# Kernel optimization log

Measured on AMD Instinct MI355X. Metric: run time of the kernel, lower is better.

Reference implementation:

```python
import jax, jax.numpy as jnp
import numpy as np

A, B, K, P, STRIDE, ITERS = 32, 32, 3, 4, 2, 3
PSIZE = P * P
EPS = 1e-8


def add_patches(x):
    # x: (b, h, w, A*PSIZE) -> (b*oh*ow, K*K*A, PSIZE)
    b, h, w, c = x.shape
    oh = (h - K) // STRIDE + 1
    ow = (w - K) // STRIDE + 1
    idx = jnp.arange(oh) * STRIDE  # same for w since h == w here
    idx = idx[:, None] + jnp.arange(K)[None, :]          # (oh, K)
    p = x[:, idx]                                        # (b, oh, K, w, c)
    p = p[:, :, :, idx]                                  # (b, oh, K, ow, K, c)
    p = jnp.transpose(p, (0, 1, 3, 2, 4, 5))             # (b, oh, ow, K, K, c)
    p = p.reshape(b * oh * ow, K * K * A, PSIZE)
    return p, oh, ow


def transform_view(p_in, weights):
    # p_in: (N, K*K*A, PSIZE); weights: (K*K*A, B, P, P)
    N = p_in.shape[0]
    x = p_in.reshape(N, K * K * A, P, P)
    # pose matmul per (input capsule i, output type j): x[n,i] @ w[i,j]
    v = jnp.einsum('nipr,ijrq->nijpq', x, weights)       # (N, KKA, B, P, P)
    return v.reshape(N, K * K * A, B, PSIZE)


def squash(p):
    n2 = jnp.sum(p * p, axis=-1, keepdims=True)
    return p * n2 / (1.0 + n2) / jnp.sqrt(n2 + EPS)


def dynamic_routing(v, iters):
    # v: (N, KKA, B, PSIZE); inverted dynamic routing: softmax over input capsules
    N, KKA, Bt, _ = v.shape
    logits = jnp.zeros((N, KKA, Bt, 1), dtype=v.dtype)
    p = None
    for i in range(iters):
        r = jax.nn.softmax(logits, axis=1)               # route over input capsules
        p = squash(jnp.sum(r * v, axis=1, keepdims=True))  # (N,1,B,PSIZE)
        if i < iters - 1:
            logits = logits + jnp.sum(v * p, axis=-1, keepdims=True)
    return p[:, 0]                                       # (N, B, PSIZE)


def setup_inputs() -> dict:
    key = jax.random.key(0)
    k1, k2 = jax.random.split(key)
    x = jax.random.normal(k1, (2, 32, 32, A * PSIZE), dtype=jnp.float32)
    weights = jax.random.normal(k2, (K * K * A, B, P, P), dtype=jnp.float32)
    return {"x": x, "weights": weights}


def reference(x, weights):
    b = x.shape[0]
    p_in, oh, ow = add_patches(x)
    v = transform_view(p_in, weights)                    # (b*oh*ow, KKA, B, PSIZE)
    p_out = dynamic_routing(v, ITERS)                    # (b*oh*ow, B, PSIZE)
    return p_out.reshape(b, oh, ow, B * PSIZE)
```

## Files before the change

### kernel.cpp

```cpp
#include <hip/hip_runtime.h>


#define OH 15
#define OW 15
#define NITERS 3
#define EPS_ 1e-8f

#define XT_ELEMS (2 * 32 * 32 * 512)
#define WT_ELEMS (32 * 5 * 64 * 16)

typedef float v2f __attribute__((ext_vector_type(2)));

__device__ __forceinline__ v2f pfma(float a, v2f b, v2f c) {
    return __builtin_elementwise_fma((v2f){a, a}, b, c);
}
__device__ __forceinline__ float b_lo(unsigned int u) {
    union { unsigned int i; float f; } c; c.i = u << 16; return c.f;
}
__device__ __forceinline__ float b_hi(unsigned int u) {
    union { unsigned int i; float f; } c; c.i = u & 0xFFFF0000u; return c.f;
}
__device__ __forceinline__ unsigned short f2bf(float f) {
    union { float f; unsigned int i; } c; c.f = f;
    return (unsigned short)((c.i + 0x7FFFu + ((c.i >> 16) & 1u)) >> 16);
}

__global__ __launch_bounds__(256) void cast_x_kernel(
    const float* __restrict__ x, unsigned short* __restrict__ xt)
{
    const int tid = blockIdx.x * 256 + threadIdx.x;
    xt[tid] = f2bf(x[tid]);
}

__global__ __launch_bounds__(256) void permute_w_kernel(
    const float* __restrict__ w, unsigned short* __restrict__ wt)
{
    const int tid = blockIdx.x * 256 + threadIdx.x;
    const int j  = tid / 5120;
    const int r  = tid - j * 5120;
    const int k  = r >> 10;
    const int L  = (r >> 4) & 63;
    const int e  = r & 15;
    const int i  = L + 64 * k;
    wt[tid] = (i < 288) ? f2bf(w[(size_t)i * 512 + j * 16 + e]) : (unsigned short)0;
}

template <bool PERM>
__global__ __launch_bounds__(64, 3) void convcaps_kernel(
    const void* __restrict__ xp,
    const void* __restrict__ wp_,
    float* __restrict__ out)
{
    const int blk  = blockIdx.x;
    const int n    = blk >> 5;
    const int j    = blk & 31;
    const int lane = threadIdx.x;

    const int batch = n / (OH * OW);
    const int rem   = n - batch * OH * OW;
    const int oy    = rem / OW;
    const int ox    = rem - oy * OW;

    const bool has5 = (lane < 32);

    v2f v[5][8];
    float logit[5] = {0.f, 0.f, 0.f, 0.f, 0.f};

#pragma unroll
    for (int k = 0; k < 5; ++k) {
        if (k == 4 && !has5) {
#pragma unroll
            for (int m = 0; m < 8; ++m) v[4][m] = (v2f){0.f, 0.f};
        } else {
            const int i  = lane + 64 * k;
            const int a  = i & 31;
            const int kw = (i >> 5) % 3;
            const int kh = i / 96;
            const int h  = oy * 2 + kh;
            const int wc = ox * 2 + kw;
            const int pixel = (batch * 32 + h) * 32 + wc;

            float xr[16];
            v2f wr2[4][2];
            if (PERM) {
                const uint4* xb = reinterpret_cast<const uint4*>(
                    (const unsigned short*)xp + ((size_t)pixel * 512 + a * 16));
                uint4 u0 = xb[0], u1 = xb[1];
                xr[0]=b_lo(u0.x); xr[1]=b_hi(u0.x); xr[2]=b_lo(u0.y); xr[3]=b_hi(u0.y);
                xr[4]=b_lo(u0.z); xr[5]=b_hi(u0.z); xr[6]=b_lo(u0.w); xr[7]=b_hi(u0.w);
                xr[8]=b_lo(u1.x); xr[9]=b_hi(u1.x); xr[10]=b_lo(u1.y); xr[11]=b_hi(u1.y);
                xr[12]=b_lo(u1.z); xr[13]=b_hi(u1.z); xr[14]=b_lo(u1.w); xr[15]=b_hi(u1.w);
                const uint4* wb = reinterpret_cast<const uint4*>(
                    (const unsigned short*)wp_ + (((size_t)j * 5 + k) * 64 + lane) * 16);
                uint4 q0 = wb[0], q1 = wb[1];
                wr2[0][0] = (v2f){b_lo(q0.x), b_hi(q0.x)};
                wr2[0][1] = (v2f){b_lo(q0.y), b_hi(q0.y)};
                wr2[1][0] = (v2f){b_lo(q0.z), b_hi(q0.z)};
                wr2[1][1] = (v2f){b_lo(q0.w), b_hi(q0.w)};
                wr2[2][0] = (v2f){b_lo(q1.x), b_hi(q1.x)};
                wr2[2][1] = (v2f){b_lo(q1.y), b_hi(q1.y)};
                wr2[3][0] = (v2f){b_lo(q1.z), b_hi(q1.z)};
                wr2[3][1] = (v2f){b_lo(q1.w), b_hi(q1.w)};
            } else {
                const float4* xv = reinterpret_cast<const float4*>(
                    (const float*)xp + ((size_t)pixel * 512 + a * 16));
                float4 x0 = xv[0], x1 = xv[1], x2 = xv[2], x3 = xv[3];
                float t_[16] = { x0.x,x0.y,x0.z,x0.w, x1.x,x1.y,x1.z,x1.w,
                                 x2.x,x2.y,x2.z,x2.w, x3.x,x3.y,x3.z,x3.w };
#pragma unroll
                for (int e = 0; e < 16; ++e) xr[e] = t_[e];
                const float4* wq = reinterpret_cast<const float4*>(
                    (const float*)wp_ + ((size_t)i * 32 + j) * 16);
                float4 w0 = wq[0], w1 = wq[1], w2 = wq[2], w3 = wq[3];
                wr2[0][0]=(v2f){w0.x,w0.y}; wr2[0][1]=(v2f){w0.z,w0.w};
                wr2[1][0]=(v2f){w1.x,w1.y}; wr2[1][1]=(v2f){w1.z,w1.w};
                wr2[2][0]=(v2f){w2.x,w2.y}; wr2[2][1]=(v2f){w2.z,w2.w};
                wr2[3][0]=(v2f){w3.x,w3.y}; wr2[3][1]=(v2f){w3.z,w3.w};
            }

#pragma unroll
            for (int p = 0; p < 4; ++p) {
#pragma unroll
                for (int qq = 0; qq < 2; ++qq) {
                    v2f acc = (v2f){0.f, 0.f};
                    acc = pfma(xr[p*4+0], wr2[0][qq], acc);
                    acc = pfma(xr[p*4+1], wr2[1][qq], acc);
                    acc = pfma(xr[p*4+2], wr2[2][qq], acc);
                    acc = pfma(xr[p*4+3], wr2[3][qq], acc);
                    v[k][p*2+qq] = acc;
                }
            }
        }
    }

#pragma unroll
    for (int it = 0; it < NITERS; ++it) {
        v2f c2[8];
        float se_loc;
        if (it == 0) {
#pragma unroll
            for (int m = 0; m < 8; ++m)
                c2[m] = v[0][m] + v[1][m] + v[2][m] + v[3][m] + v[4][m];
            se_loc = 0.f;
        } else {
            const float e0 = __expf(logit[0]), e1 = __expf(logit[1]);
            const float e2 = __expf(logit[2]), e3 = __expf(logit[3]);
            const float e4 = __expf(logit[4]);
#pragma unroll
            for (int m = 0; m < 8; ++m)
                c2[m] = pfma(e0, v[0][m],
                        pfma(e1, v[1][m],
                        pfma(e2, v[2][m],
                        pfma(e3, v[3][m],
                        pfma(e4, v[4][m], (v2f){0.f, 0.f})))));
            se_loc = e0 + e1 + e2 + e3 + (has5 ? e4 : 0.f);
        }

        float c[16];
#pragma unroll
        for (int m = 0; m < 8; ++m) { c[2*m] = c2[m].x; c[2*m+1] = c2[m].y; }

        float seR = se_loc;
        float s8[8];
        {
            const bool b = lane & 1;
#pragma unroll
            for (int m = 0; m < 8; ++m) {
                float send = b ? c[2*m]   : c[2*m+1];
                float keep = b ? c[2*m+1] : c[2*m];
                s8[m] = keep + __shfl_xor(send, 1);
            }
            seR += __shfl_xor(seR, 1);
        }
        float s4[4];
        {
            const bool b = (lane >> 1) & 1;
#pragma unroll
            for (int m = 0; m < 4; ++m) {
                float send = b ? s8[2*m]   : s8[2*m+1];
                float keep = b ? s8[2*m+1] : s8[2*m];
                s4[m] = keep + __shfl_xor(send, 2);
            }
            seR += __shfl_xor(seR, 2);
        }
        float s2v[2];
        {
            const bool b = (lane >> 2) & 1;
#pragma unroll
            for (int m = 0; m < 2; ++m) {
                float send = b ? s4[2*m]   : s4[2*m+1];
                float keep = b ? s4[2*m+1] : s4[2*m];
                s2v[m] = keep + __shfl_xor(send, 4);
            }
            seR += __shfl_xor(seR, 4);
        }
        float s1;
        {
            const bool b = (lane >> 3) & 1;
            float send = b ? s2v[0] : s2v[1];
            float keep = b ? s2v[1] : s2v[0];
            s1 = keep + __shfl_xor(send, 8);
            seR += __shfl_xor(seR, 8);
        }
        s1 += __shfl_xor(s1, 16);  seR += __shfl_xor(seR, 16);
        s1 += __shfl_xor(s1, 32);  seR += __shfl_xor(seR, 32);

        const float s = (it == 0) ? s1 * (1.0f / 288.0f) : s1 / seR;

        float t2 = s * s;
        t2 += __shfl_xor(t2, 1);
        t2 += __shfl_xor(t2, 2);
        t2 += __shfl_xor(t2, 4);
        t2 += __shfl_xor(t2, 8);
        const float n2 = t2;
        const float scale = n2 / ((1.0f + n2) * sqrtf(n2 + EPS_));
        const float pval = s * scale;

        if (it < NITERS - 1) {
            float p[16];
#pragma unroll
            for (int q = 0; q < 16; ++q) p[q] = __shfl(pval, q);
            v2f p2[8];
#pragma unroll
            for (int m = 0; m < 8; ++m) p2[m] = (v2f){p[2*m], p[2*m+1]};
#pragma unroll
            for (int k = 0; k < 5; ++k) {
                v2f acc = (v2f){0.f, 0.f};
#pragma unroll
                for (int m = 0; m < 8; ++m)
                    acc = __builtin_elementwise_fma(v[k][m], p2[m], acc);
                logit[k] += acc.x + acc.y;
            }
        } else {
            if (lane < 16)
                out[(size_t)n * 512 + j * 16 + lane] = pval;
        }
    }
}

extern "C" void kernel_launch(void* const* d_in, const int* in_sizes, int n_in,
                              void* d_out, int out_size, void* d_ws, size_t ws_size,
                              hipStream_t stream) {
    const float* x = (const float*)d_in[0];
    const float* w = (const float*)d_in[1];
    float* out = (float*)d_out;
    const int nblocks = 450 * 32;

    const size_t need = (size_t)(XT_ELEMS + WT_ELEMS) * sizeof(unsigned short);
    if (d_ws != nullptr && ws_size >= need) {
        unsigned short* xt = (unsigned short*)d_ws;
        unsigned short* wt = xt + XT_ELEMS;
        cast_x_kernel<<<XT_ELEMS / 256, 256, 0, stream>>>(x, xt);
        permute_w_kernel<<<WT_ELEMS / 256, 256, 0, stream>>>(w, wt);
        convcaps_kernel<true><<<nblocks, 64, 0, stream>>>(xt, wt, out);
    } else {
        convcaps_kernel<false><<<nblocks, 64, 0, stream>>>(x, w, out);
    }
}
```

Baseline: 86.32 us.

## Recompute capsule votes per routing iteration, merge staging kernels, use 4-wave blocks

```diff
diff --git a/kernel.cpp b/kernel.cpp
--- a/kernel.cpp
+++ b/kernel.cpp
@@ -3,7 +3,6 @@
 
 #define OH 15
 #define OW 15
-#define NITERS 3
 #define EPS_ 1e-8f
 
 #define XT_ELEMS (2 * 32 * 32 * 512)
@@ -25,36 +24,39 @@
     return (unsigned short)((c.i + 0x7FFFu + ((c.i >> 16) & 1u)) >> 16);
 }
 
-__global__ __launch_bounds__(256) void cast_x_kernel(
-    const float* __restrict__ x, unsigned short* __restrict__ xt)
+__global__ __launch_bounds__(256) void stage_kernel(
+    const float* __restrict__ x, const float* __restrict__ w,
+    unsigned short* __restrict__ xt, unsigned short* __restrict__ wt)
 {
     const int tid = blockIdx.x * 256 + threadIdx.x;
-    xt[tid] = f2bf(x[tid]);
-}
-
-__global__ __launch_bounds__(256) void permute_w_kernel(
-    const float* __restrict__ w, unsigned short* __restrict__ wt)
-{
-    const int tid = blockIdx.x * 256 + threadIdx.x;
-    const int j  = tid / 5120;
-    const int r  = tid - j * 5120;
-    const int k  = r >> 10;
-    const int L  = (r >> 4) & 63;
-    const int e  = r & 15;
-    const int i  = L + 64 * k;
-    wt[tid] = (i < 288) ? f2bf(w[(size_t)i * 512 + j * 16 + e]) : (unsigned short)0;
+    if (tid < XT_ELEMS) {
+        xt[tid] = f2bf(x[tid]);
+    } else {
+        const int t2 = tid - XT_ELEMS;
+        const int j  = t2 / 5120;
+        const int r  = t2 - j * 5120;
+        const int k  = r >> 10;
+        const int L  = (r >> 4) & 63;
+        const int e  = r & 15;
+        const int i  = L + 64 * k;
+        wt[t2] = (i < 288) ? f2bf(w[(size_t)i * 512 + j * 16 + e])
+                           : (unsigned short)0;
+    }
 }
 
 template <bool PERM>
-__global__ __launch_bounds__(64, 3) void convcaps_kernel(
+__global__ __launch_bounds__(256, 5) void convcaps_kernel(
     const void* __restrict__ xp,
     const void* __restrict__ wp_,
     float* __restrict__ out)
 {
     const int blk  = blockIdx.x;
-    const int n    = blk >> 5;
-    const int j    = blk & 31;
-    const int lane = threadIdx.x;
+    const int n    = blk >> 3;
+    const int jg   = blk & 7;
+    const int t    = threadIdx.x;
+    const int wv   = t >> 6;
+    const int lane = t & 63;
+    const int j    = jg * 4 + wv;
 
     const int batch = n / (OH * OW);
     const int rem   = n - batch * OH * OW;
@@ -63,35 +65,48 @@
 
     const bool has5 = (lane < 32);
 
-    v2f v[5][8];
+    int xoff[5], woff[5];
+#pragma unroll
+    for (int k = 0; k < 5; ++k) {
+        const int i  = lane + 64 * k;
+        const int a  = i & 31;
+        const int kw = (i >> 5) % 3;
+        const int kh = i / 96;
+        const int h  = oy * 2 + kh;
+        const int wc = ox * 2 + kw;
+        const int pixel = (batch * 32 + h) * 32 + wc;
+        xoff[k] = pixel * 512 + a * 16;
+        woff[k] = PERM ? (((j * 5 + k) * 64 + lane) * 16)
+                       : ((i * 32 + j) * 16);
+    }
+
     float logit[5] = {0.f, 0.f, 0.f, 0.f, 0.f};
-
-#pragma unroll
-    for (int k = 0; k < 5; ++k) {
-        if (k == 4 && !has5) {
-#pragma unroll
-            for (int m = 0; m < 8; ++m) v[4][m] = (v2f){0.f, 0.f};
-        } else {
-            const int i  = lane + 64 * k;
-            const int a  = i & 31;
-            const int kw = (i >> 5) % 3;
-            const int kh = i / 96;
-            const int h  = oy * 2 + kh;
-            const int wc = ox * 2 + kw;
-            const int pixel = (batch * 32 + h) * 32 + wc;
+    v2f p2[8];
+    float outval = 0.f;
+
+#pragma unroll
+    for (int it = 0; it < 3; ++it) {
+        v2f c2[8];
+#pragma unroll
+        for (int m = 0; m < 8; ++m) c2[m] = (v2f){0.f, 0.f};
+        float se_loc = 0.f;
+
+#pragma unroll
+        for (int k = 0; k < 5; ++k) {
+            if (k == 4 && !has5) continue;
 
             float xr[16];
             v2f wr2[4][2];
             if (PERM) {
                 const uint4* xb = reinterpret_cast<const uint4*>(
-                    (const unsigned short*)xp + ((size_t)pixel * 512 + a * 16));
+                    (const unsigned short*)xp + xoff[k]);
                 uint4 u0 = xb[0], u1 = xb[1];
                 xr[0]=b_lo(u0.x); xr[1]=b_hi(u0.x); xr[2]=b_lo(u0.y); xr[3]=b_hi(u0.y);
                 xr[4]=b_lo(u0.z); xr[5]=b_hi(u0.z); xr[6]=b_lo(u0.w); xr[7]=b_hi(u0.w);
                 xr[8]=b_lo(u1.x); xr[9]=b_hi(u1.x); xr[10]=b_lo(u1.y); xr[11]=b_hi(u1.y);
                 xr[12]=b_lo(u1.z); xr[13]=b_hi(u1.z); xr[14]=b_lo(u1.w); xr[15]=b_hi(u1.w);
                 const uint4* wb = reinterpret_cast<const uint4*>(
-                    (const unsigned short*)wp_ + (((size_t)j * 5 + k) * 64 + lane) * 16);
+                    (const unsigned short*)wp_ + woff[k]);
                 uint4 q0 = wb[0], q1 = wb[1];
                 wr2[0][0] = (v2f){b_lo(q0.x), b_hi(q0.x)};
                 wr2[0][1] = (v2f){b_lo(q0.y), b_hi(q0.y)};
@@ -103,14 +118,14 @@
                 wr2[3][1] = (v2f){b_lo(q1.w), b_hi(q1.w)};
             } else {
                 const float4* xv = reinterpret_cast<const float4*>(
-                    (const float*)xp + ((size_t)pixel * 512 + a * 16));
+                    (const float*)xp + xoff[k]);
                 float4 x0 = xv[0], x1 = xv[1], x2 = xv[2], x3 = xv[3];
                 float t_[16] = { x0.x,x0.y,x0.z,x0.w, x1.x,x1.y,x1.z,x1.w,
                                  x2.x,x2.y,x2.z,x2.w, x3.x,x3.y,x3.z,x3.w };
 #pragma unroll
                 for (int e = 0; e < 16; ++e) xr[e] = t_[e];
                 const float4* wq = reinterpret_cast<const float4*>(
-                    (const float*)wp_ + ((size_t)i * 32 + j) * 16);
+                    (const float*)wp_ + woff[k]);
                 float4 w0 = wq[0], w1 = wq[1], w2 = wq[2], w3 = wq[3];
                 wr2[0][0]=(v2f){w0.x,w0.y}; wr2[0][1]=(v2f){w0.z,w0.w};
                 wr2[1][0]=(v2f){w1.x,w1.y}; wr2[1][1]=(v2f){w1.z,w1.w};
@@ -118,42 +133,34 @@
                 wr2[3][0]=(v2f){w3.x,w3.y}; wr2[3][1]=(v2f){w3.z,w3.w};
             }
 
-#pragma unroll
-            for (int p = 0; p < 4; ++p) {
+            v2f vk[8];
+#pragma unroll
+            for (int pp = 0; pp < 4; ++pp) {
 #pragma unroll
                 for (int qq = 0; qq < 2; ++qq) {
                     v2f acc = (v2f){0.f, 0.f};
-                    acc = pfma(xr[p*4+0], wr2[0][qq], acc);
-                    acc = pfma(xr[p*4+1], wr2[1][qq], acc);
-                    acc = pfma(xr[p*4+2], wr2[2][qq], acc);
-                    acc = pfma(xr[p*4+3], wr2[3][qq], acc);
-                    v[k][p*2+qq] = acc;
+                    acc = pfma(xr[pp*4+0], wr2[0][qq], acc);
+                    acc = pfma(xr[pp*4+1], wr2[1][qq], acc);
+                    acc = pfma(xr[pp*4+2], wr2[2][qq], acc);
+                    acc = pfma(xr[pp*4+3], wr2[3][qq], acc);
+                    vk[pp*2+qq] = acc;
                 }
             }
-        }
-    }
-
-#pragma unroll
-    for (int it = 0; it < NITERS; ++it) {
-        v2f c2[8];
-        float se_loc;
-        if (it == 0) {
-#pragma unroll
-            for (int m = 0; m < 8; ++m)
-                c2[m] = v[0][m] + v[1][m] + v[2][m] + v[3][m] + v[4][m];
-            se_loc = 0.f;
-        } else {
-            const float e0 = __expf(logit[0]), e1 = __expf(logit[1]);
-            const float e2 = __expf(logit[2]), e3 = __expf(logit[3]);
-            const float e4 = __expf(logit[4]);
-#pragma unroll
-            for (int m = 0; m < 8; ++m)
-                c2[m] = pfma(e0, v[0][m],
-                        pfma(e1, v[1][m],
-                        pfma(e2, v[2][m],
-                        pfma(e3, v[3][m],
-                        pfma(e4, v[4][m], (v2f){0.f, 0.f})))));
-            se_loc = e0 + e1 + e2 + e3 + (has5 ? e4 : 0.f);
+
+            if (it == 0) {
+#pragma unroll
+                for (int m = 0; m < 8; ++m) c2[m] += vk[m];
+            } else {
+                v2f dd = (v2f){0.f, 0.f};
+#pragma unroll
+                for (int m = 0; m < 8; ++m)
+                    dd = __builtin_elementwise_fma(vk[m], p2[m], dd);
+                logit[k] += dd.x + dd.y;
+                const float e = __expf(logit[k]);
+                se_loc += e;
+#pragma unroll
+                for (int m = 0; m < 8; ++m) c2[m] = pfma(e, vk[m], c2[m]);
+            }
         }
 
         float c[16];
@@ -170,7 +177,7 @@
                 float keep = b ? c[2*m+1] : c[2*m];
                 s8[m] = keep + __shfl_xor(send, 1);
             }
-            seR += __shfl_xor(seR, 1);
+            if (it > 0) seR += __shfl_xor(seR, 1);
         }
         float s4[4];
         {
@@ -181,7 +188,7 @@
                 float keep = b ? s8[2*m+1] : s8[2*m];
                 s4[m] = keep + __shfl_xor(send, 2);
             }
-            seR += __shfl_xor(seR, 2);
+            if (it > 0) seR += __shfl_xor(seR, 2);
         }
         float s2v[2];
         {
@@ -192,7 +199,7 @@
                 float keep = b ? s4[2*m+1] : s4[2*m];
                 s2v[m] = keep + __shfl_xor(send, 4);
             }
-            seR += __shfl_xor(seR, 4);
+            if (it > 0) seR += __shfl_xor(seR, 4);
         }
         float s1;
         {
@@ -200,10 +207,10 @@
             float send = b ? s2v[0] : s2v[1];
             float keep = b ? s2v[1] : s2v[0];
             s1 = keep + __shfl_xor(send, 8);
-            seR += __shfl_xor(seR, 8);
-        }
-        s1 += __shfl_xor(s1, 16);  seR += __shfl_xor(seR, 16);
-        s1 += __shfl_xor(s1, 32);  seR += __shfl_xor(seR, 32);
+            if (it > 0) seR += __shfl_xor(seR, 8);
+        }
+        s1 += __shfl_xor(s1, 16);  if (it > 0) seR += __shfl_xor(seR, 16);
+        s1 += __shfl_xor(s1, 32);  if (it > 0) seR += __shfl_xor(seR, 32);
 
         const float s = (it == 0) ? s1 * (1.0f / 288.0f) : s1 / seR;
 
@@ -216,26 +223,17 @@
         const float scale = n2 / ((1.0f + n2) * sqrtf(n2 + EPS_));
         const float pval = s * scale;
 
-        if (it < NITERS - 1) {
-            float p[16];
-#pragma unroll
-            for (int q = 0; q < 16; ++q) p[q] = __shfl(pval, q);
-            v2f p2[8];
-#pragma unroll
-            for (int m = 0; m < 8; ++m) p2[m] = (v2f){p[2*m], p[2*m+1]};
-#pragma unroll
-            for (int k = 0; k < 5; ++k) {
-                v2f acc = (v2f){0.f, 0.f};
-#pragma unroll
-                for (int m = 0; m < 8; ++m)
-                    acc = __builtin_elementwise_fma(v[k][m], p2[m], acc);
-                logit[k] += acc.x + acc.y;
-            }
+        if (it < 2) {
+#pragma unroll
+            for (int m = 0; m < 8; ++m)
+                p2[m] = (v2f){__shfl(pval, 2*m), __shfl(pval, 2*m + 1)};
         } else {
-            if (lane < 16)
-                out[(size_t)n * 512 + j * 16 + lane] = pval;
-        }
-    }
+            outval = pval;
+        }
+    }
+
+    if (lane < 16)
+        out[(size_t)n * 512 + j * 16 + lane] = outval;
 }
 
 extern "C" void kernel_launch(void* const* d_in, const int* in_sizes, int n_in,
@@ -244,16 +242,15 @@
     const float* x = (const float*)d_in[0];
     const float* w = (const float*)d_in[1];
     float* out = (float*)d_out;
-    const int nblocks = 450 * 32;
+    const int nblocks = 450 * 8;
 
     const size_t need = (size_t)(XT_ELEMS + WT_ELEMS) * sizeof(unsigned short);
     if (d_ws != nullptr && ws_size >= need) {
         unsigned short* xt = (unsigned short*)d_ws;
         unsigned short* wt = xt + XT_ELEMS;
-        cast_x_kernel<<<XT_ELEMS / 256, 256, 0, stream>>>(x, xt);
-        permute_w_kernel<<<WT_ELEMS / 256, 256, 0, stream>>>(w, wt);
-        convcaps_kernel<true><<<nblocks, 64, 0, stream>>>(xt, wt, out);
+        stage_kernel<<<(XT_ELEMS + WT_ELEMS) / 256, 256, 0, stream>>>(x, w, xt, wt);
+        convcaps_kernel<true><<<nblocks, 256, 0, stream>>>(xt, wt, out);
     } else {
-        convcaps_kernel<false><<<nblocks, 64, 0, stream>>>(x, w, out);
-    }
-}
+        convcaps_kernel<false><<<nblocks, 256, 0, stream>>>(x, w, out);
+    }
+}
```

After: 115.4 us. 1.34x slower.
